# Optimization experiments

Hardware: AMD Instinct MI355X
Metric: run time of the kernel (lower is better)

## Reference

```python
import jax, jax.numpy as jnp
import numpy as np

B, T, S, D, V, PAD = 8, 4095, 2048, 300, 32000, 1


def setup_inputs() -> dict:
    key = jax.random.key(0)
    k1, k2, k3, k4 = jax.random.split(key, 4)
    # tokens in [2, V) so none collide with padding_idx
    x = jax.random.randint(k1, (B, T), 2, V, dtype=jnp.int64)
    # first S nodes are leaves: indices (i, i); remaining T-S are internal spans hi > lo
    leaf = jnp.arange(S, dtype=jnp.int64)
    leaf_pairs = jnp.broadcast_to(jnp.stack([leaf, leaf], -1)[None], (B, S, 2))
    n_int = T - S
    lo = jax.random.randint(k2, (B, n_int), 0, S - 1, dtype=jnp.int64)
    span = jax.random.randint(k3, (B, n_int), 1, 64, dtype=jnp.int64)
    hi = jnp.minimum(lo + span, S - 1)
    int_pairs = jnp.stack([lo, hi], -1)
    indices = jnp.concatenate([leaf_pairs, int_pairs], axis=1)  # [B, T, 2]
    W = jax.random.normal(k4, (V, D), jnp.float32) * 0.02
    W = W.at[PAD].set(0.0)  # padding_idx row is zero, as in nn.Embedding
    return {"x": x, "indices": indices, "W": W}


def reference(x, indices, W):
    b, t = x.shape
    s = (t + 1) // 2
    # _retrieve_leaves: left-pack tokens whose (lo==hi) and token != PAD
    is_leaf = (indices[:, :, 0] == indices[:, :, 1]) & (x != PAD)  # [b,t]
    pos = jnp.cumsum(is_leaf.astype(jnp.int32), axis=1) - 1       # packed slot per leaf
    safe_pos = jnp.where(is_leaf, pos, s)                          # out-of-range -> dropped
    leaves = jnp.full((b, s), PAD, dtype=x.dtype)
    leaves = leaves.at[jnp.arange(b)[:, None], safe_pos].set(x, mode="drop")  # [b,s]
    # interval mask: lo <= r <= hi  (computed as (r>=lo) XOR (r>hi), as in source)
    r = jnp.arange(s)[None, None, :]                               # [1,1,s]
    mask = ((r >= indices[:, :, 0:1]) ^ (r > indices[:, :, 1:2])).astype(W.dtype)  # [b,t,s]
    emb = W[leaves]                                                # [b,s,D]
    denom = jnp.maximum(mask.sum(-1, keepdims=True), 1.0)          # [b,t,1]
    # same math as (mask[...,None] * emb[:,None]).sum(2), without the [b,t,s,D] tensor
    out = jnp.einsum("bts,bsd->btd", mask, emb) / denom
    return out
```

## Files before the change

kernel.cpp:

```cpp
#include <hip/hip_runtime.h>


#define BB 8
#define TT 4095
#define SS 2048
#define DD 300
#define PADIDX 1
#define CHUNK 32
#define NC (SS / CHUNK)
#define NTB 320

__global__ __launch_bounds__(512) void leaves_kernel(const int* __restrict__ x,
                                                     const int* __restrict__ idx,
                                                     int* __restrict__ leaves) {
    int b = blockIdx.x, tid = threadIdx.x;
    int lane = tid & 63, w = tid >> 6;
    __shared__ int wcnt[8];
    __shared__ int sbase;
    if (tid == 0) sbase = 0;
    __syncthreads();
    const int* xb = x + b * TT;
    const int* ib = idx + b * 2 * TT;
    for (int t0 = 0; t0 < TT; t0 += 512) {
        int t = t0 + tid;
        bool leaf = false;
        int xv = 0;
        if (t < TT) {
            xv = xb[t];
            leaf = (ib[2 * t] == ib[2 * t + 1]) && (xv != PADIDX);
        }
        unsigned long long bal = __ballot(leaf);
        if (lane == 0) wcnt[w] = __popcll(bal);
        __syncthreads();
        int off = sbase;
        for (int i = 0; i < w; ++i) off += wcnt[i];
        int pos = off + __popcll(bal & ((1ull << lane) - 1ull));
        if (leaf && pos < SS) leaves[b * SS + pos] = xv;
        __syncthreads();
        if (tid == 0) {
            int s = 0;
            for (int i = 0; i < 8; ++i) s += wcnt[i];
            sbase += s;
        }
        __syncthreads();
    }
    for (int i = sbase + tid; i < SS; i += 512) leaves[b * SS + i] = PADIDX;
}

__global__ __launch_bounds__(NTB) void csum_kernel(const int* __restrict__ leaves,
                                                   const float* __restrict__ W,
                                                   float* __restrict__ csum) {
    int blk = blockIdx.x;
    int b = blk >> 6, c = blk & (NC - 1);
    int tid = threadIdx.x;
    __shared__ int lf[CHUNK];
    if (tid < CHUNK) lf[tid] = leaves[b * SS + c * CHUNK + tid];
    __syncthreads();
    int d = tid;
    if (d >= DD) return;
    float acc = 0.f;
#pragma unroll 8
    for (int i = 0; i < CHUNK; ++i) acc += W[lf[i] * DD + d];
    csum[(b * NC + c) * DD + d] = acc;
}

__global__ __launch_bounds__(NTB) void buildP_kernel(const int* __restrict__ leaves,
                                                     const float* __restrict__ W,
                                                     const float* __restrict__ csum,
                                                     float* __restrict__ P) {
    int blk = blockIdx.x;
    int b = blk >> 6, c = blk & (NC - 1);
    int tid = threadIdx.x;
    __shared__ int lf[CHUNK];
    if (tid < CHUNK) lf[tid] = leaves[b * SS + c * CHUNK + tid];
    __syncthreads();
    int d = tid;
    if (d >= DD) return;

    float base = 0.f;
#pragma unroll 4
    for (int cc = 0; cc < c; ++cc) base += csum[(b * NC + cc) * DD + d];

    float v[CHUNK];
#pragma unroll
    for (int i = 0; i < CHUNK; ++i) v[i] = W[lf[i] * DD + d];

    float* Pb = P + (size_t)b * (SS + 1) * DD;
    int s0 = c * CHUNK;
    float run = base;
#pragma unroll
    for (int i = 0; i < CHUNK; ++i) {
        Pb[(s0 + i) * DD + d] = run;
        run += v[i];
    }
    if (c == NC - 1) Pb[SS * DD + d] = run;
}

__global__ __launch_bounds__(NTB) void out_kernel(const int* __restrict__ idx,
                                                  const float* __restrict__ P,
                                                  float* __restrict__ out) {
    int tid = threadIdx.x;
    int r = tid / 80, j = tid - r * 80;
    int base_bt = blockIdx.x * 16 + r;
    const float4* P4 = (const float4*)P;
    float4* out4 = (float4*)out;
#pragma unroll
    for (int it = 0; it < 4; ++it) {
        int bt = base_bt + it * 4;
        if (bt >= BB * TT || j >= 75) continue;
        int b = bt / TT;
        int lo = idx[2 * bt], hi = idx[2 * bt + 1];
        int u = hi + 1;
        int a = min(lo, u), e = max(lo, u);
        a = max(0, min(a, SS));
        e = max(0, min(e, SS));
        int cnt = e - a;
        float inv = 1.0f / (float)(cnt > 0 ? cnt : 1);
        size_t pb = (size_t)b * (SS + 1);
        float4 ve = P4[(pb + e) * 75 + j];
        float4 va = P4[(pb + a) * 75 + j];
        float4 o;
        o.x = (ve.x - va.x) * inv;
        o.y = (ve.y - va.y) * inv;
        o.z = (ve.z - va.z) * inv;
        o.w = (ve.w - va.w) * inv;
        out4[(size_t)bt * 75 + j] = o;
    }
}

extern "C" void kernel_launch(void* const* d_in, const int* in_sizes, int n_in,
                              void* d_out, int out_size, void* d_ws, size_t ws_size,
                              hipStream_t stream) {
    const int* x = (const int*)d_in[0];
    const int* idx = (const int*)d_in[1];
    const float* W = (const float*)d_in[2];
    float* out = (float*)d_out;

    char* ws = (char*)d_ws;
    int* leaves = (int*)ws;
    float* csum = (float*)(ws + 65536);
    float* P = (float*)(ws + 65536 + 614400);

    leaves_kernel<<<BB, 512, 0, stream>>>(x, idx, leaves);
    csum_kernel<<<BB * NC, NTB, 0, stream>>>(leaves, W, csum);
    buildP_kernel<<<BB * NC, NTB, 0, stream>>>(leaves, W, csum, P);
    out_kernel<<<(BB * TT + 15) / 16, NTB, 0, stream>>>(idx, P, out);
}
```

Measured before the change: 123.3 us.

## Pin each batch to one XCD, prefetch leaf loads, use nontemporal output stores

Block indices in csum, buildP and out kernels are remapped so the batch index is the fastest-varying part (blk & 7). With round-robin block dispatch across the 8 XCDs, each batch's prefix-sum table P then stays in a single XCD's L2, which is meant to cut cross-XCD traffic on the gather reads. The leaves kernel now issues all eight token and index loads up front, before the ballot and scan loop, to hide load latency. The output is written with nontemporal stores so it does not evict P from cache. The index remap relies on the assumed dispatch order, and the prefetch uses extra registers.

```diff
diff --git a/kernel.cpp b/kernel.cpp
--- a/kernel.cpp
+++ b/kernel.cpp
@@ -10,6 +10,8 @@
 #define NC (SS / CHUNK)
 #define NTB 320
 
+typedef float f4 __attribute__((ext_vector_type(4)));
+
 __global__ __launch_bounds__(512) void leaves_kernel(const int* __restrict__ x,
                                                      const int* __restrict__ idx,
                                                      int* __restrict__ leaves) {
@@ -18,24 +20,31 @@
     __shared__ int wcnt[8];
     __shared__ int sbase;
     if (tid == 0) sbase = 0;
-    __syncthreads();
     const int* xb = x + b * TT;
     const int* ib = idx + b * 2 * TT;
-    for (int t0 = 0; t0 < TT; t0 += 512) {
-        int t = t0 + tid;
-        bool leaf = false;
-        int xv = 0;
+
+    int xv[8];
+    bool lf8[8];
+#pragma unroll
+    for (int k = 0; k < 8; ++k) {
+        int t = tid + k * 512;
+        xv[k] = 0;
+        lf8[k] = false;
         if (t < TT) {
-            xv = xb[t];
-            leaf = (ib[2 * t] == ib[2 * t + 1]) && (xv != PADIDX);
+            xv[k] = xb[t];
+            lf8[k] = (ib[2 * t] == ib[2 * t + 1]) && (xv[k] != PADIDX);
         }
-        unsigned long long bal = __ballot(leaf);
+    }
+    __syncthreads();
+#pragma unroll
+    for (int k = 0; k < 8; ++k) {
+        unsigned long long bal = __ballot(lf8[k]);
         if (lane == 0) wcnt[w] = __popcll(bal);
         __syncthreads();
         int off = sbase;
         for (int i = 0; i < w; ++i) off += wcnt[i];
         int pos = off + __popcll(bal & ((1ull << lane) - 1ull));
-        if (leaf && pos < SS) leaves[b * SS + pos] = xv;
+        if (lf8[k] && pos < SS) leaves[b * SS + pos] = xv[k];
         __syncthreads();
         if (tid == 0) {
             int s = 0;
@@ -51,7 +60,7 @@
                                                    const float* __restrict__ W,
                                                    float* __restrict__ csum) {
     int blk = blockIdx.x;
-    int b = blk >> 6, c = blk & (NC - 1);
+    int b = blk & 7, c = blk >> 3;
     int tid = threadIdx.x;
     __shared__ int lf[CHUNK];
     if (tid < CHUNK) lf[tid] = leaves[b * SS + c * CHUNK + tid];
@@ -69,7 +78,7 @@
                                                      const float* __restrict__ csum,
                                                      float* __restrict__ P) {
     int blk = blockIdx.x;
-    int b = blk >> 6, c = blk & (NC - 1);
+    int b = blk & 7, c = blk >> 3;
     int tid = threadIdx.x;
     __shared__ int lf[CHUNK];
     if (tid < CHUNK) lf[tid] = leaves[b * SS + c * CHUNK + tid];
@@ -101,30 +110,26 @@
                                                   float* __restrict__ out) {
     int tid = threadIdx.x;
     int r = tid / 80, j = tid - r * 80;
-    int base_bt = blockIdx.x * 16 + r;
-    const float4* P4 = (const float4*)P;
-    float4* out4 = (float4*)out;
+    int b = blockIdx.x & 7;
+    int g = blockIdx.x >> 3;
+    const f4* P4 = (const f4*)(P + (size_t)b * (SS + 1) * DD);
+    f4* out4 = (f4*)out;
+    const int* ixb = idx + 2 * b * TT;
 #pragma unroll
     for (int it = 0; it < 4; ++it) {
-        int bt = base_bt + it * 4;
-        if (bt >= BB * TT || j >= 75) continue;
-        int b = bt / TT;
-        int lo = idx[2 * bt], hi = idx[2 * bt + 1];
+        int lr = g * 16 + r + it * 4;
+        if (lr >= TT || j >= 75) continue;
+        int lo = ixb[2 * lr], hi = ixb[2 * lr + 1];
         int u = hi + 1;
         int a = min(lo, u), e = max(lo, u);
         a = max(0, min(a, SS));
         e = max(0, min(e, SS));
         int cnt = e - a;
         float inv = 1.0f / (float)(cnt > 0 ? cnt : 1);
-        size_t pb = (size_t)b * (SS + 1);
-        float4 ve = P4[(pb + e) * 75 + j];
-        float4 va = P4[(pb + a) * 75 + j];
-        float4 o;
-        o.x = (ve.x - va.x) * inv;
-        o.y = (ve.y - va.y) * inv;
-        o.z = (ve.z - va.z) * inv;
-        o.w = (ve.w - va.w) * inv;
-        out4[(size_t)bt * 75 + j] = o;
+        f4 ve = P4[(size_t)e * 75 + j];
+        f4 va = P4[(size_t)a * 75 + j];
+        f4 o = (ve - va) * inv;
+        __builtin_nontemporal_store(o, &out4[((size_t)b * TT + lr) * 75 + j]);
     }
 }
 
```

After: 116.0 us. -6.0%, faster.
